# Optimization experiments

Measured on AMD Instinct MI355X. Metric: run time of the kernel, lower is better.

The kernel has to match this reference:

```python
import jax, jax.numpy as jnp
import numpy as np

N_HEADS = 16
N_KV_HEADS = 4
HEAD_DIM = 128
ROPE_THETA = 1000000.0

def setup_inputs() -> dict:
    key = jax.random.key(0)
    ks = jax.random.split(key, 5)
    B, T, D = 2, 2048, 2048
    s = 1.0 / np.sqrt(D)
    return {
        'x':  jax.random.normal(ks[0], (B, T, D), dtype=jnp.float32),
        'wq': jax.random.normal(ks[1], (D, N_HEADS * HEAD_DIM), dtype=jnp.float32) * s,
        'wk': jax.random.normal(ks[2], (D, N_KV_HEADS * HEAD_DIM), dtype=jnp.float32) * s,
        'wv': jax.random.normal(ks[3], (D, N_KV_HEADS * HEAD_DIM), dtype=jnp.float32) * s,
        'wo': jax.random.normal(ks[4], (N_HEADS * HEAD_DIM, D), dtype=jnp.float32) * s,
    }

def _rope_cos_sin(T, dtype):
    # build_rope_cache: inv_freq over half the head dim, cos/sin of shape [T, HEAD_DIM]
    half = HEAD_DIM // 2
    inv_freq = 1.0 / (ROPE_THETA ** (jnp.arange(0, half, dtype=jnp.float32) * 2.0 / HEAD_DIM))
    ang = jnp.arange(T, dtype=jnp.float32)[:, None] * inv_freq[None, :]  # [T, half]
    ang = jnp.concatenate([ang, ang], axis=-1)  # [T, HEAD_DIM]
    return jnp.cos(ang).astype(dtype), jnp.sin(ang).astype(dtype)

def _rotate_half(u):
    u1, u2 = jnp.split(u, 2, axis=-1)
    return jnp.concatenate([-u2, u1], axis=-1)

def _apply_rotary(h, cos, sin):
    # h: [B, H, T, hd]; cos/sin: [T, hd]
    return h * cos[None, None, :, :] + _rotate_half(h) * sin[None, None, :, :]

def _attention(x, wq, wk, wv, wo):
    B, T, D = x.shape
    dtype = x.dtype
    scale = HEAD_DIM ** -0.5
    # QKV projection + split heads -> [B, H, T, hd]
    qh = (x @ wq).reshape(B, T, N_HEADS, HEAD_DIM).transpose(0, 2, 1, 3)
    kh = (x @ wk).reshape(B, T, N_KV_HEADS, HEAD_DIM).transpose(0, 2, 1, 3)
    vh = (x @ wv).reshape(B, T, N_KV_HEADS, HEAD_DIM).transpose(0, 2, 1, 3)
    # RoPE
    cos, sin = _rope_cos_sin(T, dtype)
    qh = _apply_rotary(qh, cos, sin)
    kh = _apply_rotary(kh, cos, sin)
    # GQA: repeat kv heads
    rep = N_HEADS // N_KV_HEADS
    kh = jnp.repeat(kh, rep, axis=1)
    vh = jnp.repeat(vh, rep, axis=1)
    # eager attention: full score matrix [B, H, T, T]
    scores = jnp.einsum('bhtd,bhsd->bhts', qh, kh) * scale
    causal = jnp.tril(jnp.ones((T, T), dtype=bool))
    neg = jnp.asarray(jnp.finfo(jnp.float32).min, dtype=jnp.float32)
    scores = jnp.where(causal[None, None, :, :], scores.astype(jnp.float32), neg)
    probs = jax.nn.softmax(scores, axis=-1).astype(dtype)
    out = jnp.einsum('bhts,bhsd->bhtd', probs, vh)
    y = out.transpose(0, 2, 1, 3).reshape(B, T, N_HEADS * HEAD_DIM)  # merge heads
    return y @ wo

def reference(x, wq, wk, wv, wo):
    return _attention(x, wq, wk, wv, wo)
```

## Files before the change

### kernel.cpp

```cpp
#include <hip/hip_runtime.h>


#define T_SZ 2048
#define D_SZ 2048
#define BT   4096

typedef __attribute__((ext_vector_type(8))) short bf16x8;
typedef __attribute__((ext_vector_type(4))) float f32x4;

__device__ __forceinline__ unsigned short f2b(float f) {
  unsigned u = __float_as_uint(f);
  u = (u + 0x7fffu + ((u >> 16) & 1u)) >> 16;
  return (unsigned short)u;
}
__device__ __forceinline__ float b2f(unsigned short h) {
  return __uint_as_float(((unsigned)h) << 16);
}

#if __has_builtin(__builtin_amdgcn_exp2f)
__device__ __forceinline__ float exp2_fast(float x) { return __builtin_amdgcn_exp2f(x); }
#else
__device__ __forceinline__ float exp2_fast(float x) {
  float r; asm("v_exp_f32 %0, %1" : "=v"(r) : "v"(x)); return r;
}
#endif

__device__ __forceinline__ void async_ld16(const void* g, void* l) {
  __builtin_amdgcn_global_load_lds(
      (const __attribute__((address_space(1))) void*)g,
      (__attribute__((address_space(3))) void*)l, 16, 0, 0);
}

union Pack8 { unsigned short us[8]; uint4 v; };

__global__ __launch_bounds__(256) void cast_f32_bf16(
    const float* __restrict__ in, unsigned short* __restrict__ out) {
  int i = (blockIdx.x * 256 + threadIdx.x) * 4;
  float4 v = *(const float4*)(in + i);
  ushort4 o;
  o.x = f2b(v.x); o.y = f2b(v.y); o.z = f2b(v.z); o.w = f2b(v.w);
  *(ushort4*)(out + i) = o;
}

__global__ __launch_bounds__(256) void cast_transpose_all(
    const float* __restrict__ wq, const float* __restrict__ wk,
    const float* __restrict__ wv, const float* __restrict__ wo,
    unsigned short* __restrict__ qkvT, unsigned short* __restrict__ woT) {
  __shared__ float tile[64][68];
  int bx = blockIdx.x;
  const float* W; unsigned short* WT; int N, nb;
  if (bx < 32)      { W = wq; WT = qkvT;                         N = 2048; nb = bx; }
  else if (bx < 40) { W = wk; WT = qkvT + (size_t)2048 * 2048;   N = 512;  nb = bx - 32; }
  else if (bx < 48) { W = wv; WT = qkvT + (size_t)2560 * 2048;   N = 512;  nb = bx - 40; }
  else              { W = wo; WT = woT;                          N = 2048; nb = bx - 48; }
  const int K = 2048;
  int n0 = nb * 64, k0 = blockIdx.y * 64;
  int t = threadIdx.x;
#pragma unroll
  for (int i = 0; i < 4; i++) {
    int c = t + 256 * i;
    int r = c >> 4, cc = c & 15;
    float4 v = *(const float4*)(W + (size_t)(k0 + r) * N + n0 + cc * 4);
    tile[r][cc * 4 + 0] = v.x; tile[r][cc * 4 + 1] = v.y;
    tile[r][cc * 4 + 2] = v.z; tile[r][cc * 4 + 3] = v.w;
  }
  __syncthreads();
#pragma unroll
  for (int i = 0; i < 2; i++) {
    int c = t + 256 * i;
    int n = c >> 3, kc = c & 7;
    Pack8 p;
#pragma unroll
    for (int j = 0; j < 8; j++) p.us[j] = f2b(tile[kc * 8 + j][n]);
    *(uint4*)(WT + (size_t)(n0 + n) * K + k0 + kc * 8) = p.v;
  }
}

template <int OUT_BF16>
__global__ __launch_bounds__(256) void gemm_bt(
    const unsigned short* __restrict__ A, const unsigned short* __restrict__ Bt,
    void* __restrict__ C, int M, int N, int K) {
  __shared__ unsigned short As[2][128 * 32];
  __shared__ unsigned short Bs[2][128 * 32];
  int t = threadIdx.x;
  int lane = t & 63, wave = t >> 6;
  int m0 = blockIdx.y * 128, n0 = blockIdx.x * 128;
  int wm = (wave >> 1) * 64, wn = (wave & 1) * 64;
  int fr = lane & 15, fq = lane >> 4;

  int srow = wave * 32 + (lane >> 2);
  int scol = (lane & 3) * 8;
  const unsigned short* Ag = A + (size_t)(m0 + srow) * K + scol;
  const unsigned short* Bg = Bt + (size_t)(n0 + srow) * K + scol;

  auto stage = [&](int k0_, int bf) {
#pragma unroll
    for (int j = 0; j < 2; j++) {
      async_ld16(Ag + (size_t)j * 16 * K + k0_, &As[bf][wave * 1024 + j * 512]);
      async_ld16(Bg + (size_t)j * 16 * K + k0_, &Bs[bf][wave * 1024 + j * 512]);
    }
  };

  f32x4 acc[4][4];
#pragma unroll
  for (int mi = 0; mi < 4; mi++)
#pragma unroll
    for (int ni = 0; ni < 4; ni++) acc[mi][ni] = (f32x4){0.f, 0.f, 0.f, 0.f};

  stage(0, 0);
  int cur = 0;
  for (int k0 = 0; k0 < K; k0 += 32) {
    if (k0 + 32 < K) {
      stage(k0 + 32, cur ^ 1);
      asm volatile("s_waitcnt vmcnt(4)" ::: "memory");
    } else {
      asm volatile("s_waitcnt vmcnt(0)" ::: "memory");
    }
    __builtin_amdgcn_s_barrier();
    asm volatile("" ::: "memory");
    bf16x8 a[4], b[4];
#pragma unroll
    for (int mi = 0; mi < 4; mi++)
      a[mi] = *(const bf16x8*)(&As[cur][(wm + 16 * mi + fr) * 32 + fq * 8]);
#pragma unroll
    for (int ni = 0; ni < 4; ni++)
      b[ni] = *(const bf16x8*)(&Bs[cur][(wn + 16 * ni + fr) * 32 + fq * 8]);
#pragma unroll
    for (int mi = 0; mi < 4; mi++)
#pragma unroll
      for (int ni = 0; ni < 4; ni++)
        acc[mi][ni] = __builtin_amdgcn_mfma_f32_16x16x32_bf16(
            a[mi], b[ni], acc[mi][ni], 0, 0, 0);
    asm volatile("s_waitcnt lgkmcnt(0)" ::: "memory");
    __builtin_amdgcn_s_barrier();
    asm volatile("" ::: "memory");
    cur ^= 1;
  }
#pragma unroll
  for (int mi = 0; mi < 4; mi++)
#pragma unroll
    for (int ni = 0; ni < 4; ni++)
#pragma unroll
      for (int r = 0; r < 4; r++) {
        int row = m0 + wm + 16 * mi + fq * 4 + r;
        int col = n0 + wn + 16 * ni + fr;
        float v = acc[mi][ni][r];
        if (OUT_BF16)
          ((unsigned short*)C)[(size_t)row * N + col] = f2b(v);
        else
          ((float*)C)[(size_t)row * N + col] = v;
      }
}

template <int LOGH, int STRIDE, int SCALE_Q>
__global__ __launch_bounds__(256) void rope_inplace(unsigned short* __restrict__ X) {
  int p = blockIdx.x * 256 + threadIdx.x;
  int d = p & 63;
  int h = (p >> 6) & ((1 << LOGH) - 1);
  int row = p >> (6 + LOGH);
  int tpos = row & (T_SZ - 1);
  size_t base = (size_t)row * STRIDE + h * 128 + d;
  float u1 = b2f(X[base]), u2 = b2f(X[base + 64]);
  float inv = expf(-(float)d * 0.21586735246819178f);
  float ang = (float)tpos * inv;
  float c = cosf(ang), s = sinf(ang);
  float o1 = u1 * c - u2 * s;
  float o2 = u2 * c + u1 * s;
  if (SCALE_Q) { o1 *= 0.08838834764831845f; o2 *= 0.08838834764831845f; }
  X[base]      = f2b(o1);
  X[base + 64] = f2b(o2);
}

__global__ __launch_bounds__(256) void transpose_v(
    const unsigned short* __restrict__ V ,
    unsigned short* __restrict__ VT) {
  __shared__ unsigned short tile[64][72];
  int t0 = blockIdx.x * 64;
  int n0 = blockIdx.y * 64;
  int bk = blockIdx.z;
  int b = bk >> 2, kvh = bk & 3;
  int t = threadIdx.x;
#pragma unroll
  for (int i = 0; i < 2; i++) {
    int c = t + 256 * i;
    int r = c >> 3, cc = c & 7;
    *(uint4*)&tile[r][cc * 8] = *(const uint4*)(
        V + (size_t)(b * T_SZ + t0 + r) * 3072 + kvh * 128 + n0 + cc * 8);
  }
  __syncthreads();
#pragma unroll
  for (int i = 0; i < 2; i++) {
    int c = t + 256 * i;
    int n = c >> 3, tc = c & 7;
    Pack8 p;
#pragma unroll
    for (int j = 0; j < 8; j++) p.us[j] = tile[tc * 8 + j][n];
    *(uint4*)(VT + ((size_t)bk * 128 + n0 + n) * T_SZ + t0 + tc * 8) = p.v;
  }
}

__global__ __launch_bounds__(512) void attn(
    const unsigned short* __restrict__ Q,
    const unsigned short* __restrict__ KV,
    const unsigned short* __restrict__ VT,
    unsigned short* __restrict__ O) {
  __shared__ unsigned short Ks[2][64 * 128];
  __shared__ unsigned short Vt[128 * 64];
  __shared__ unsigned short Ps[8][16 * 76];
  int qt = blockIdx.z ? blockIdx.x : 15 - blockIdx.x;
  int h = blockIdx.y, b = blockIdx.z;
  int kvh = h >> 2;
  int t = threadIdx.x, lane = t & 63, w = t >> 6;
  int fr = lane & 15, fq = lane >> 4;
  int rsw = fr & 7;

  bf16x8 qf[4];
#pragma unroll
  for (int kk = 0; kk < 4; kk++)
    qf[kk] = *(const bf16x8*)(
        Q + (size_t)(b * T_SZ + qt * 128 + w * 16 + fr) * 3072 +
        h * 128 + kk * 32 + fq * 8);

  const unsigned short* Kg = KV + (size_t)b * T_SZ * 3072 + kvh * 128;
  const unsigned short* Vg = VT + (size_t)(b * 4 + kvh) * 128 * T_SZ;

  int k_lr = lane >> 4, k_ls = lane & 15;
  int v_lr = lane >> 3, v_ls = lane & 7;

  auto stage_k = [&](int kt_, int bf) {
#pragma unroll
    for (int j = 0; j < 2; j++) {
      int row = w * 8 + j * 4 + k_lr;
      async_ld16(Kg + (size_t)(kt_ * 64 + row) * 3072 + ((k_ls ^ (row & 7)) << 3),
                 &Ks[bf][(w * 8 + j * 4) * 128]);
    }
  };
  auto stage_v = [&](int kt_) {
#pragma unroll
    for (int j = 0; j < 2; j++) {
      int row = w * 16 + j * 8 + v_lr;
      async_ld16(Vg + (size_t)row * T_SZ + kt_ * 64 + ((v_ls ^ (row & 7)) << 3),
                 &Vt[(w * 16 + j * 8) * 64]);
    }
  };

  stage_k(0, 0);
  stage_v(0);

  {
    const float QSCL = 0.08838834764831845f * 1.4426950408889634f;
    float tposf = (float)(qt * 128 + w * 16 + fr);
#pragma unroll
    for (int kk = 0; kk < 2; kk++)
#pragma unroll
      for (int j = 0; j < 8; j++) {
        int d = kk * 32 + (fq << 3) + j;
        float u1 = b2f((unsigned short)qf[kk][j]);
        float u2 = b2f((unsigned short)qf[kk + 2][j]);
        float inv = __expf(-(float)d * 0.21586735246819178f);
        float ang = tposf * inv, c, s;
        __sincosf(ang, &s, &c);
        qf[kk][j]     = (short)f2b((u1 * c - u2 * s) * QSCL);
        qf[kk + 2][j] = (short)f2b((u2 * c + u1 * s) * QSCL);
      }
  }

  f32x4 o[8];
#pragma unroll
  for (int i = 0; i < 8; i++) o[i] = (f32x4){0.f, 0.f, 0.f, 0.f};
  float mrow = -1e30f, lrow = 0.f;
  int qg = qt * 128 + w * 16 + fr;
  int nkt = 2 * qt + 2;

  int cur = 0;
  for (int kt = 0; kt < nkt; kt++) {
    if (kt + 1 < nkt) {
      stage_k(kt + 1, cur ^ 1);
      asm volatile("s_waitcnt vmcnt(2)" ::: "memory");
    } else {
      asm volatile("s_waitcnt vmcnt(0)" ::: "memory");
    }
    __builtin_amdgcn_s_barrier();
    asm volatile("" ::: "memory");

    const unsigned short* KsC = Ks[cur];

    f32x4 s[4];
    __builtin_amdgcn_s_setprio(1);
#pragma unroll
    for (int nn = 0; nn < 4; nn++) {
      s[nn] = (f32x4){0.f, 0.f, 0.f, 0.f};
#pragma unroll
      for (int kk = 0; kk < 4; kk++) {
        bf16x8 kf = *(const bf16x8*)(
            KsC + (nn * 16 + fr) * 128 + ((((kk << 2) + fq) ^ rsw) << 3));
        s[nn] = __builtin_amdgcn_mfma_f32_16x16x32_bf16(kf, qf[kk], s[nn], 0, 0, 0);
      }
    }
    __builtin_amdgcn_s_setprio(0);
    if (kt * 64 + 63 > qg) {
#pragma unroll
      for (int nn = 0; nn < 4; nn++)
#pragma unroll
        for (int r = 0; r < 4; r++) {
          int kvg = kt * 64 + nn * 16 + fq * 4 + r;
          if (kvg > qg) s[nn][r] = -1e30f;
        }
    }
    f32x4 t4;
#pragma unroll
    for (int r = 0; r < 4; r++)
      t4[r] = fmaxf(fmaxf(s[0][r], s[1][r]), fmaxf(s[2][r], s[3][r]));
    float mx = fmaxf(fmaxf(t4[0], t4[1]), fmaxf(t4[2], t4[3]));
    mx = fmaxf(mx, __shfl_xor(mx, 16, 64));
    mx = fmaxf(mx, __shfl_xor(mx, 32, 64));
    if (__any(mx > mrow + 8.0f)) {
      float mnew = fmaxf(mrow, mx);
      float alpha = exp2_fast(mrow - mnew);
      lrow *= alpha;
#pragma unroll
      for (int nt = 0; nt < 8; nt++)
#pragma unroll
        for (int r = 0; r < 4; r++) o[nt][r] *= alpha;
      mrow = mnew;
    }
    float sum = 0.f;
#pragma unroll
    for (int nn = 0; nn < 4; nn++) {
      ushort4 pk;
      float p0 = exp2_fast(s[nn][0] - mrow); pk.x = f2b(p0);
      float p1 = exp2_fast(s[nn][1] - mrow); pk.y = f2b(p1);
      float p2 = exp2_fast(s[nn][2] - mrow); pk.z = f2b(p2);
      float p3 = exp2_fast(s[nn][3] - mrow); pk.w = f2b(p3);
      sum += (p0 + p1) + (p2 + p3);
      *(ushort4*)(Ps[w] + fr * 76 + nn * 16 + fq * 4) = pk;
    }
    lrow += sum;
    __builtin_amdgcn_s_setprio(1);
#pragma unroll
    for (int kk = 0; kk < 2; kk++) {
      bf16x8 pf = *(const bf16x8*)(Ps[w] + fr * 76 + kk * 32 + fq * 8);
#pragma unroll
      for (int nt = 0; nt < 8; nt++) {
        bf16x8 vf = *(const bf16x8*)(
            Vt + (nt * 16 + fr) * 64 + ((((kk << 2) + fq) ^ rsw) << 3));
        o[nt] = __builtin_amdgcn_mfma_f32_16x16x32_bf16(vf, pf, o[nt], 0, 0, 0);
      }
    }
    __builtin_amdgcn_s_setprio(0);
    asm volatile("s_waitcnt lgkmcnt(0)" ::: "memory");
    __builtin_amdgcn_s_barrier();
    asm volatile("" ::: "memory");
    if (kt + 1 < nkt) stage_v(kt + 1);
    cur ^= 1;
  }
  float lsum = lrow;
  lsum += __shfl_xor(lsum, 16, 64);
  lsum += __shfl_xor(lsum, 32, 64);
  float linv = 1.f / lsum;
  int rowg = b * T_SZ + qt * 128 + w * 16 + fr;
#pragma unroll
  for (int nt = 0; nt < 8; nt++) {
    ushort4 ov;
    ov.x = f2b(o[nt][0] * linv);
    ov.y = f2b(o[nt][1] * linv);
    ov.z = f2b(o[nt][2] * linv);
    ov.w = f2b(o[nt][3] * linv);
    *(ushort4*)(O + (size_t)rowg * 2048 + h * 128 + nt * 16 + fq * 4) = ov;
  }
}

extern "C" void kernel_launch(void* const* d_in, const int* in_sizes, int n_in,
                              void* d_out, int out_size, void* d_ws, size_t ws_size,
                              hipStream_t stream) {
  const float* x  = (const float*)d_in[0];
  const float* wq = (const float*)d_in[1];
  const float* wk = (const float*)d_in[2];
  const float* wv = (const float*)d_in[3];
  const float* wo = (const float*)d_in[4];
  float* out = (float*)d_out;

  unsigned short* xb   = (unsigned short*)d_ws;
  unsigned short* wqT  = xb   + (size_t)4096 * 2048;
  unsigned short* woT  = wqT  + (size_t)3072 * 2048;
  unsigned short* QKVb = woT  + (size_t)2048 * 2048;
  unsigned short* VTb  = QKVb + (size_t)4096 * 3072;
  unsigned short* AOb  = VTb  + (size_t)4096 * 512;

  cast_f32_bf16<<<8192, 256, 0, stream>>>(x, xb);
  cast_transpose_all<<<dim3(80, 32), 256, 0, stream>>>(wq, wk, wv, wo, wqT, woT);

  gemm_bt<1><<<dim3(24, 32), 256, 0, stream>>>(xb, wqT, QKVb, 4096, 3072, 2048);

  rope_inplace<2, 3072, 0><<<4096, 256, 0, stream>>>(QKVb + 2048);
  transpose_v<<<dim3(32, 2, 8), 256, 0, stream>>>(QKVb + 2560, VTb);

  attn<<<dim3(16, 16, 2), 512, 0, stream>>>(QKVb, QKVb + 2048, VTb, AOb);

  gemm_bt<0><<<dim3(16, 32), 256, 0, stream>>>(AOb, woT, (void*)out, 4096, 2048, 2048);
}
```

Baseline: 299.5 us.

## Single-buffer K tile via register prefetch to cut LDS and raise occupancy

```diff
diff --git a/kernel.cpp b/kernel.cpp
--- a/kernel.cpp
+++ b/kernel.cpp
@@ -199,12 +199,12 @@
   }
 }
 
-__global__ __launch_bounds__(512) void attn(
+__global__ __launch_bounds__(512, 6) void attn(
     const unsigned short* __restrict__ Q,
     const unsigned short* __restrict__ KV,
     const unsigned short* __restrict__ VT,
     unsigned short* __restrict__ O) {
-  __shared__ unsigned short Ks[2][64 * 128];
+  __shared__ unsigned short Ks[64 * 128];
   __shared__ unsigned short Vt[128 * 64];
   __shared__ unsigned short Ps[8][16 * 76];
   int qt = blockIdx.z ? blockIdx.x : 15 - blockIdx.x;
@@ -227,13 +227,19 @@
   int k_lr = lane >> 4, k_ls = lane & 15;
   int v_lr = lane >> 3, v_ls = lane & 7;
 
-  auto stage_k = [&](int kt_, int bf) {
+  uint4 kreg[2];
+  auto load_k = [&](int kt_) {
 #pragma unroll
     for (int j = 0; j < 2; j++) {
       int row = w * 8 + j * 4 + k_lr;
-      async_ld16(Kg + (size_t)(kt_ * 64 + row) * 3072 + ((k_ls ^ (row & 7)) << 3),
-                 &Ks[bf][(w * 8 + j * 4) * 128]);
-    }
+      kreg[j] = *(const uint4*)(
+          Kg + (size_t)(kt_ * 64 + row) * 3072 + ((k_ls ^ (row & 7)) << 3));
+    }
+  };
+  auto write_k = [&]() {
+#pragma unroll
+    for (int j = 0; j < 2; j++)
+      *(uint4*)&Ks[(w * 8 + j * 4) * 128 + lane * 8] = kreg[j];
   };
   auto stage_v = [&](int kt_) {
 #pragma unroll
@@ -244,8 +250,7 @@
     }
   };
 
-  stage_k(0, 0);
-  stage_v(0);
+  load_k(0);
 
   {
     const float QSCL = 0.08838834764831845f * 1.4426950408889634f;
@@ -265,6 +270,11 @@
       }
   }
 
+  asm volatile("s_waitcnt vmcnt(0)" ::: "memory");
+  write_k();
+  asm volatile("s_waitcnt lgkmcnt(0)" ::: "memory");
+  stage_v(0);
+
   f32x4 o[8];
 #pragma unroll
   for (int i = 0; i < 8; i++) o[i] = (f32x4){0.f, 0.f, 0.f, 0.f};
@@ -272,10 +282,9 @@
   int qg = qt * 128 + w * 16 + fr;
   int nkt = 2 * qt + 2;
 
-  int cur = 0;
   for (int kt = 0; kt < nkt; kt++) {
     if (kt + 1 < nkt) {
-      stage_k(kt + 1, cur ^ 1);
+      load_k(kt + 1);
       asm volatile("s_waitcnt vmcnt(2)" ::: "memory");
     } else {
       asm volatile("s_waitcnt vmcnt(0)" ::: "memory");
@@ -283,8 +292,6 @@
     __builtin_amdgcn_s_barrier();
     asm volatile("" ::: "memory");
 
-    const unsigned short* KsC = Ks[cur];
-
     f32x4 s[4];
     __builtin_amdgcn_s_setprio(1);
 #pragma unroll
@@ -293,7 +300,7 @@
 #pragma unroll
       for (int kk = 0; kk < 4; kk++) {
         bf16x8 kf = *(const bf16x8*)(
-            KsC + (nn * 16 + fr) * 128 + ((((kk << 2) + fq) ^ rsw) << 3));
+            Ks + (nn * 16 + fr) * 128 + ((((kk << 2) + fq) ^ rsw) << 3));
         s[nn] = __builtin_amdgcn_mfma_f32_16x16x32_bf16(kf, qf[kk], s[nn], 0, 0, 0);
       }
     }
@@ -351,8 +358,12 @@
     asm volatile("s_waitcnt lgkmcnt(0)" ::: "memory");
     __builtin_amdgcn_s_barrier();
     asm volatile("" ::: "memory");
-    if (kt + 1 < nkt) stage_v(kt + 1);
-    cur ^= 1;
+    if (kt + 1 < nkt) {
+      asm volatile("s_waitcnt vmcnt(0)" ::: "memory");
+      write_k();
+      asm volatile("s_waitcnt lgkmcnt(0)" ::: "memory");
+      stage_v(kt + 1);
+    }
   }
   float lsum = lrow;
   lsum += __shfl_xor(lsum, 16, 64);
```

New measurement: 429.0 us. 43.2% more time.

## Merge prep kernels into fewer launches and swizzle GEMM tile order

Applied to the files above, without the earlier changes.

```diff
diff --git a/kernel.cpp b/kernel.cpp
--- a/kernel.cpp
+++ b/kernel.cpp
@@ -33,29 +33,30 @@
 
 union Pack8 { unsigned short us[8]; uint4 v; };
 
-__global__ __launch_bounds__(256) void cast_f32_bf16(
-    const float* __restrict__ in, unsigned short* __restrict__ out) {
-  int i = (blockIdx.x * 256 + threadIdx.x) * 4;
-  float4 v = *(const float4*)(in + i);
-  ushort4 o;
-  o.x = f2b(v.x); o.y = f2b(v.y); o.z = f2b(v.z); o.w = f2b(v.w);
-  *(ushort4*)(out + i) = o;
-}
-
-__global__ __launch_bounds__(256) void cast_transpose_all(
+__global__ __launch_bounds__(256) void prep(
+    const float* __restrict__ x, unsigned short* __restrict__ xb,
     const float* __restrict__ wq, const float* __restrict__ wk,
     const float* __restrict__ wv, const float* __restrict__ wo,
     unsigned short* __restrict__ qkvT, unsigned short* __restrict__ woT) {
   __shared__ float tile[64][68];
-  int bx = blockIdx.x;
+  int bid = blockIdx.x, t = threadIdx.x;
+  if (bid < 8192) {
+    int i = (bid * 256 + t) * 4;
+    float4 v = *(const float4*)(x + i);
+    ushort4 o;
+    o.x = f2b(v.x); o.y = f2b(v.y); o.z = f2b(v.z); o.w = f2b(v.w);
+    *(ushort4*)(xb + i) = o;
+    return;
+  }
+  int rem = bid - 8192;
+  int bx = rem % 80, ky = rem / 80;
   const float* W; unsigned short* WT; int N, nb;
-  if (bx < 32)      { W = wq; WT = qkvT;                         N = 2048; nb = bx; }
-  else if (bx < 40) { W = wk; WT = qkvT + (size_t)2048 * 2048;   N = 512;  nb = bx - 32; }
-  else if (bx < 48) { W = wv; WT = qkvT + (size_t)2560 * 2048;   N = 512;  nb = bx - 40; }
-  else              { W = wo; WT = woT;                          N = 2048; nb = bx - 48; }
+  if (bx < 32)      { W = wq; WT = qkvT;                       N = 2048; nb = bx; }
+  else if (bx < 40) { W = wk; WT = qkvT + (size_t)2048 * 2048; N = 512;  nb = bx - 32; }
+  else if (bx < 48) { W = wv; WT = qkvT + (size_t)2560 * 2048; N = 512;  nb = bx - 40; }
+  else              { W = wo; WT = woT;                        N = 2048; nb = bx - 48; }
   const int K = 2048;
-  int n0 = nb * 64, k0 = blockIdx.y * 64;
-  int t = threadIdx.x;
+  int n0 = nb * 64, k0 = ky * 64;
 #pragma unroll
   for (int i = 0; i < 4; i++) {
     int c = t + 256 * i;
@@ -84,7 +85,11 @@
   __shared__ unsigned short Bs[2][128 * 32];
   int t = threadIdx.x;
   int lane = t & 63, wave = t >> 6;
-  int m0 = blockIdx.y * 128, n0 = blockIdx.x * 128;
+  int lin = blockIdx.y * gridDim.x + blockIdx.x;
+  int cpx = (gridDim.x * gridDim.y) >> 3;
+  int swz = (lin & 7) * cpx + (lin >> 3);
+  int bx = swz % gridDim.x, by = swz / gridDim.x;
+  int m0 = by * 128, n0 = bx * 128;
   int wm = (wave >> 1) * 64, wn = (wave & 1) * 64;
   int fr = lane & 15, fq = lane >> 4;
 
@@ -152,34 +157,32 @@
       }
 }
 
-template <int LOGH, int STRIDE, int SCALE_Q>
-__global__ __launch_bounds__(256) void rope_inplace(unsigned short* __restrict__ X) {
-  int p = blockIdx.x * 256 + threadIdx.x;
-  int d = p & 63;
-  int h = (p >> 6) & ((1 << LOGH) - 1);
-  int row = p >> (6 + LOGH);
-  int tpos = row & (T_SZ - 1);
-  size_t base = (size_t)row * STRIDE + h * 128 + d;
-  float u1 = b2f(X[base]), u2 = b2f(X[base + 64]);
-  float inv = expf(-(float)d * 0.21586735246819178f);
-  float ang = (float)tpos * inv;
-  float c = cosf(ang), s = sinf(ang);
-  float o1 = u1 * c - u2 * s;
-  float o2 = u2 * c + u1 * s;
-  if (SCALE_Q) { o1 *= 0.08838834764831845f; o2 *= 0.08838834764831845f; }
-  X[base]      = f2b(o1);
-  X[base + 64] = f2b(o2);
-}
-
-__global__ __launch_bounds__(256) void transpose_v(
+__global__ __launch_bounds__(256) void prep2(
+    unsigned short* __restrict__ Kx ,
     const unsigned short* __restrict__ V ,
     unsigned short* __restrict__ VT) {
   __shared__ unsigned short tile[64][72];
-  int t0 = blockIdx.x * 64;
-  int n0 = blockIdx.y * 64;
-  int bk = blockIdx.z;
+  int bid = blockIdx.x, t = threadIdx.x;
+  if (bid < 4096) {
+    int p = bid * 256 + t;
+    int d = p & 63;
+    int h = (p >> 6) & 3;
+    int row = p >> 8;
+    int tpos = row & (T_SZ - 1);
+    size_t base = (size_t)row * 3072 + h * 128 + d;
+    float u1 = b2f(Kx[base]), u2 = b2f(Kx[base + 64]);
+    float inv = expf(-(float)d * 0.21586735246819178f);
+    float ang = (float)tpos * inv;
+    float c = cosf(ang), s = sinf(ang);
+    Kx[base]      = f2b(u1 * c - u2 * s);
+    Kx[base + 64] = f2b(u2 * c + u1 * s);
+    return;
+  }
+  int c0 = bid - 4096;
+  int t0 = (c0 & 31) * 64;
+  int n0 = ((c0 >> 5) & 1) * 64;
+  int bk = c0 >> 6;
   int b = bk >> 2, kvh = bk & 3;
-  int t = threadIdx.x;
 #pragma unroll
   for (int i = 0; i < 2; i++) {
     int c = t + 256 * i;
@@ -387,13 +390,11 @@
   unsigned short* VTb  = QKVb + (size_t)4096 * 3072;
   unsigned short* AOb  = VTb  + (size_t)4096 * 512;
 
-  cast_f32_bf16<<<8192, 256, 0, stream>>>(x, xb);
-  cast_transpose_all<<<dim3(80, 32), 256, 0, stream>>>(wq, wk, wv, wo, wqT, woT);
+  prep<<<10752, 256, 0, stream>>>(x, xb, wq, wk, wv, wo, wqT, woT);
 
   gemm_bt<1><<<dim3(24, 32), 256, 0, stream>>>(xb, wqT, QKVb, 4096, 3072, 2048);
 
-  rope_inplace<2, 3072, 0><<<4096, 256, 0, stream>>>(QKVb + 2048);
-  transpose_v<<<dim3(32, 2, 8), 256, 0, stream>>>(QKVb + 2560, VTb);
+  prep2<<<4608, 256, 0, stream>>>(QKVb + 2048, QKVb + 2560, VTb);
 
   attn<<<dim3(16, 16, 2), 512, 0, stream>>>(QKVb, QKVb + 2048, VTb, AOb);
 
```

Result: no change. 295.0 us (-1.5%).
